# Optimization experiments

Measured on AMD Instinct MI355X. Metric: run time of the kernel, lower is better.

## Reference

```python
import jax, jax.numpy as jnp
import numpy as np

B, D_IN, D_OUT = 64, 1024, 1024

def setup_inputs() -> dict:
    key = jax.random.key(0)
    ks = jax.random.split(key, 7)
    return {
        "a_mean": jax.random.normal(ks[0], (B, D_IN), jnp.float32),
        "a_cov": jax.random.normal(ks[1], (B, D_IN, D_IN), jnp.float32),
        "weight": jax.random.normal(ks[2], (D_OUT, D_IN), jnp.float32) / np.sqrt(D_IN),
        "bias": jax.random.normal(ks[3], (D_OUT,), jnp.float32),
        "w_kfacs_A": jax.random.normal(ks[4], (D_IN, D_IN), jnp.float32) / np.sqrt(D_IN),
        "w_kfacs_B": jax.random.normal(ks[5], (D_OUT, D_OUT), jnp.float32) / np.sqrt(D_OUT),
        "b_cov": jax.random.normal(ks[6], (D_OUT, D_OUT), jnp.float32),
    }

def reference(a_mean, a_cov, weight, bias, w_kfacs_A, w_kfacs_B, b_cov):
    # h_mean = a_mean @ W^T + b
    h_mean = a_mean @ weight.T + bias  # [B, D_out]
    # Kron term: einsum('ni,nj,kl,ij->nkl') = (a_mean_n^T A a_mean_n) * B_kl
    s = jnp.einsum('ni,ij,nj->n', a_mean, w_kfacs_A, a_mean)  # [B]
    # Trace term: einsum('nij,kl,ij->nkl') = (sum_ij a_cov_nij * A_ij) * B_kl
    t = jnp.einsum('nij,ij->n', a_cov, w_kfacs_A)  # [B]
    kron_term = (s + t)[:, None, None] * w_kfacs_B  # [B, D_out, D_out]
    # Input-cov term: W @ a_cov_n @ W^T
    wcov = jnp.einsum('ki,nij,lj->nkl', weight, a_cov, weight)  # [B, D_out, D_out]
    h_cov = kron_term + wcov + b_cov
    return (h_mean, h_cov)
```

## Files before the change

### kernel.cpp

```cpp
#include <hip/hip_runtime.h>
#include <hip/hip_bf16.h>

typedef short bf16x8 __attribute__((ext_vector_type(8)));
typedef float f32x4  __attribute__((ext_vector_type(4)));

#define KD 1024

__device__ __forceinline__ short f2bf(float f) {
  unsigned u = __builtin_bit_cast(unsigned, f);
  u += 0x7fffu + ((u >> 16) & 1u);
  return (short)(u >> 16);
}

__device__ __forceinline__ void gll16(const short* g, short* l) {
  __builtin_amdgcn_global_load_lds((const __attribute__((address_space(1))) unsigned int*)g,
                                   (__attribute__((address_space(3))) unsigned int*)l,
                                   16, 0, 0);
}

template <int MODE>
__global__ __launch_bounds__(256) void gemm_bt(
    const short* __restrict__ A, size_t a_bs,
    const short* __restrict__ B, size_t b_bs,
    float* __restrict__ out, size_t o_bs,
    short* __restrict__ tout, size_t t_bs,
    const float* __restrict__ kB, const float* __restrict__ bcv,
    const float* __restrict__ cvec, int ncv0,
    const float* __restrict__ bias, int M) {
  __shared__ short sA[128 * 32];
  __shared__ short sB[128 * 32];
  const int t = threadIdx.x;
  const int z = blockIdx.z;
  const short* Ab = A + (size_t)z * a_bs;
  const short* Bb = B + (size_t)z * b_bs;
  const int m0 = blockIdx.x * 0 + blockIdx.y * 128, n0 = blockIdx.x * 128;
  const int lane = t & 63, wv = t >> 6;
  const int wm = (wv >> 1) * 64, wn = (wv & 1) * 64;
  const int r16 = lane & 15, q = lane >> 4;

  const int srow = wv * 16 + (lane >> 2);
  const int skof = (lane & 3) * 8;
  short* lA0 = &sA[(wv * 16) * 32];
  short* lA1 = &sA[(64 + wv * 16) * 32];
  short* lB0 = &sB[(wv * 16) * 32];
  short* lB1 = &sB[(64 + wv * 16) * 32];
  const int ar0 = min(m0 + srow, M - 1);
  const int ar1 = min(m0 + 64 + srow, M - 1);
  const short* gA0 = Ab + (size_t)ar0 * KD + skof;
  const short* gA1 = Ab + (size_t)ar1 * KD + skof;
  const short* gB0 = Bb + (size_t)(n0 + srow) * KD + skof;
  const short* gB1 = Bb + (size_t)(n0 + 64 + srow) * KD + skof;

  f32x4 acc[4][4];
  const f32x4 zero4 = {0.f, 0.f, 0.f, 0.f};
#pragma unroll
  for (int i = 0; i < 4; ++i)
#pragma unroll
    for (int j = 0; j < 4; ++j) acc[i][j] = zero4;

  for (int k0 = 0; k0 < KD; k0 += 32) {
    __syncthreads();
    gll16(gA0 + k0, lA0);
    gll16(gA1 + k0, lA1);
    gll16(gB0 + k0, lB0);
    gll16(gB1 + k0, lB1);
    __syncthreads();

    bf16x8 af[4], bf[4];
#pragma unroll
    for (int i = 0; i < 4; ++i) {
      af[i] = *(const bf16x8*)&sA[(wm + i * 16 + r16) * 32 + q * 8];
      bf[i] = *(const bf16x8*)&sB[(wn + i * 16 + r16) * 32 + q * 8];
    }
#pragma unroll
    for (int mi = 0; mi < 4; ++mi)
#pragma unroll
      for (int ni = 0; ni < 4; ++ni)
        acc[mi][ni] = __builtin_amdgcn_mfma_f32_16x16x32_bf16(af[mi], bf[ni], acc[mi][ni], 0, 0, 0);
  }

  float cv = 0.f;
  if (MODE == 2) cv = cvec[ncv0 + z];
  float* ob = out ? out + (size_t)z * o_bs : nullptr;

#pragma unroll
  for (int mi = 0; mi < 4; ++mi) {
#pragma unroll
    for (int ni = 0; ni < 4; ++ni) {
      const int row0 = m0 + wm + mi * 16 + q * 4;
      const int col = n0 + wn + ni * 16 + r16;
      f32x4 a = acc[mi][ni];
      if (MODE == 0) {
        float bv = bias[col];
#pragma unroll
        for (int r = 0; r < 4; ++r)
          if (row0 + r < M) ob[(size_t)(row0 + r) * 1024 + col] = a[r] + bv;
      } else if (MODE == 1) {
        short4 s;
        s.x = f2bf(a[0]); s.y = f2bf(a[1]); s.z = f2bf(a[2]); s.w = f2bf(a[3]);
        *(short4*)(tout + (size_t)z * t_bs + (size_t)col * 1024 + row0) = s;
      } else {
#pragma unroll
        for (int r = 0; r < 4; ++r) {
          size_t idx = (size_t)(row0 + r) * 1024 + col;
          ob[idx] = a[r] + cv * kB[idx] + bcv[idx];
        }
      }
    }
  }
}

__global__ __launch_bounds__(256) void conv_acov(const float* __restrict__ a_cov,
                                                 const float* __restrict__ a_mean,
                                                 const float* __restrict__ kA,
                                                 short* __restrict__ abf,
                                                 float* __restrict__ c) {
  const int n = blockIdx.x, ch = blockIdx.y, t = threadIdx.x;
  __shared__ float sm[1024];
  for (int j = t; j < 1024; j += 256) sm[j] = a_mean[n * 1024 + j];
  __syncthreads();
  const float4 amv = ((const float4*)sm)[t];
  const size_t cb = ((size_t)n << 20);
  float acc = 0.f;
  for (int i = ch * 64; i < ch * 64 + 64; ++i) {
    float4 Av = ((const float4*)(kA + ((size_t)i << 10)))[t];
    float4 Cv = ((const float4*)(a_cov + cb + ((size_t)i << 10)))[t];
    short4 s;
    s.x = f2bf(Cv.x); s.y = f2bf(Cv.y); s.z = f2bf(Cv.z); s.w = f2bf(Cv.w);
    *(short4*)(abf + cb + ((size_t)i << 10) + t * 4) = s;
    acc += Av.x * Cv.x + Av.y * Cv.y + Av.z * Cv.z + Av.w * Cv.w;
    acc += sm[i] * (Av.x * amv.x + Av.y * amv.y + Av.z * amv.z + Av.w * amv.w);
  }
#pragma unroll
  for (int off = 32; off > 0; off >>= 1) acc += __shfl_down(acc, off);
  __shared__ float red[4];
  if ((t & 63) == 0) red[t >> 6] = acc;
  __syncthreads();
  if (t == 0) atomicAdd(&c[n], red[0] + red[1] + red[2] + red[3]);
}

__global__ __launch_bounds__(256) void convf(const float* __restrict__ src,
                                             short* __restrict__ dst, int n4) {
  int i = blockIdx.x * 256 + threadIdx.x;
  if (i < n4) {
    float4 v = ((const float4*)src)[i];
    short4 s;
    s.x = f2bf(v.x); s.y = f2bf(v.y); s.z = f2bf(v.z); s.w = f2bf(v.w);
    ((short4*)dst)[i] = s;
  }
}

extern "C" void kernel_launch(void* const* d_in, const int* in_sizes, int n_in,
                              void* d_out, int out_size, void* d_ws, size_t ws_size,
                              hipStream_t stream) {
  const float* a_mean = (const float*)d_in[0];
  const float* a_cov  = (const float*)d_in[1];
  const float* weight = (const float*)d_in[2];
  const float* bias   = (const float*)d_in[3];
  const float* kA     = (const float*)d_in[4];
  const float* kB     = (const float*)d_in[5];
  const float* b_cov  = (const float*)d_in[6];
  float* h_mean = (float*)d_out;
  float* h_cov  = h_mean + (size_t)64 * 1024;

  const size_t SLICE = (size_t)1 << 20;
  float* cvec = (float*)d_ws;
  short* Wbf  = (short*)((char*)d_ws + 4096);
  short* ambf = Wbf + SLICE;
  char*  p    = (char*)(ambf + 65536);
  const size_t need_big = (size_t)((char*)p - (char*)d_ws) + 4 * SLICE * 64;
  const bool big = ws_size >= need_big;

  short* abf, *Tt;
  if (big) {
    abf = (short*)p;
    Tt  = abf + 64 * SLICE;
  } else {
    abf = (short*)h_cov;
    Tt  = (short*)(h_cov + 64 * SLICE / 2);
  }

  hipMemsetAsync(cvec, 0, 64 * sizeof(float), stream);
  convf<<<dim3(1024), 256, 0, stream>>>(weight, Wbf, 262144);
  convf<<<dim3(64), 256, 0, stream>>>(a_mean, ambf, 16384);
  conv_acov<<<dim3(64, 16), 256, 0, stream>>>(a_cov, a_mean, kA, abf, cvec);

  gemm_bt<1><<<dim3(8, 8, 64), 256, 0, stream>>>(
      abf, SLICE, Wbf, 0, nullptr, 0, Tt, SLICE,
      nullptr, nullptr, nullptr, 0, nullptr, 1024);

  gemm_bt<0><<<dim3(8, 1, 1), 256, 0, stream>>>(
      ambf, 0, Wbf, 0, h_mean, 0, nullptr, 0,
      nullptr, nullptr, nullptr, 0, bias, 64);

  if (big) {
    gemm_bt<2><<<dim3(8, 8, 64), 256, 0, stream>>>(
        Wbf, 0, Tt, SLICE, h_cov, SLICE, nullptr, 0,
        kB, b_cov, cvec, 0, nullptr, 1024);
  } else {
    short* T63 = ambf + 65536;
    hipMemcpyAsync(T63, Tt + 63 * SLICE, SLICE * 2, hipMemcpyDeviceToDevice, stream);
    const int st[6] = {0, 32, 48, 56, 60, 62};
    const int ln[6] = {32, 16, 8, 4, 2, 1};
    for (int w = 0; w < 6; ++w) {
      gemm_bt<2><<<dim3(8, 8, ln[w]), 256, 0, stream>>>(
          Wbf, 0, Tt + (size_t)st[w] * SLICE, SLICE,
          h_cov + (size_t)st[w] * SLICE, SLICE, nullptr, 0,
          kB, b_cov, cvec, st[w], nullptr, 1024);
    }
    gemm_bt<2><<<dim3(8, 8, 1), 256, 0, stream>>>(
        Wbf, 0, T63, 0, h_cov + (size_t)63 * SLICE, 0, nullptr, 0,
        kB, b_cov, cvec, 63, nullptr, 1024);
  }
}
```

Baseline: 957.1 us.

## Add 256x256-tile double-buffered GEMM kernel with swizzled LDS for batched covariance GEMMs

Adds a new 512-thread GEMM kernel with 256x256 output tiles and a 64-wide K step. It double-buffers LDS through async global-to-LDS loads, uses XOR-swizzled LDS addressing and interleaves MFMA quarters with barriers and priority hints. Both large batched GEMMs (a_cov@W^T and W@T plus the kron/bias epilogue) use it when 128KB of dynamic LDS can be configured. It aims to raise arithmetic intensity per LDS byte and overlap loads with compute. The cost is much higher register and LDS pressure per block and fewer blocks in the grid.

```diff
diff --git a/kernel.cpp b/kernel.cpp
--- a/kernel.cpp
+++ b/kernel.cpp
@@ -33,7 +33,7 @@
   const int z = blockIdx.z;
   const short* Ab = A + (size_t)z * a_bs;
   const short* Bb = B + (size_t)z * b_bs;
-  const int m0 = blockIdx.x * 0 + blockIdx.y * 128, n0 = blockIdx.x * 128;
+  const int m0 = blockIdx.y * 128, n0 = blockIdx.x * 128;
   const int lane = t & 63, wv = t >> 6;
   const int wm = (wv >> 1) * 64, wn = (wv & 1) * 64;
   const int r16 = lane & 15, q = lane >> 4;
@@ -96,6 +96,130 @@
         for (int r = 0; r < 4; ++r)
           if (row0 + r < M) ob[(size_t)(row0 + r) * 1024 + col] = a[r] + bv;
       } else if (MODE == 1) {
+        short4 s;
+        s.x = f2bf(a[0]); s.y = f2bf(a[1]); s.z = f2bf(a[2]); s.w = f2bf(a[3]);
+        *(short4*)(tout + (size_t)z * t_bs + (size_t)col * 1024 + row0) = s;
+      } else {
+#pragma unroll
+        for (int r = 0; r < 4; ++r) {
+          size_t idx = (size_t)(row0 + r) * 1024 + col;
+          ob[idx] = a[r] + cv * kB[idx] + bcv[idx];
+        }
+      }
+    }
+  }
+}
+
+template <int MODE>
+__global__ __launch_bounds__(512, 2) void gemm256(
+    const short* __restrict__ A, size_t a_bs,
+    const short* __restrict__ B, size_t b_bs,
+    float* __restrict__ out, size_t o_bs,
+    short* __restrict__ tout, size_t t_bs,
+    const float* __restrict__ kB, const float* __restrict__ bcv,
+    const float* __restrict__ cvec, int ncv0) {
+  extern __shared__ short lds[];
+  short* ldsB = lds + 32768;
+  const int t = threadIdx.x;
+  const int z = blockIdx.z;
+  const short* Ab = A + (size_t)z * a_bs;
+  const short* Bb = B + (size_t)z * b_bs;
+  const int m0 = blockIdx.y * 256, n0 = blockIdx.x * 256;
+  const int lane = t & 63, wv = t >> 6;
+  const int wm = (wv >> 2) * 128, wn = (wv & 3) * 64;
+  const int r16 = lane & 15, q = lane >> 4;
+  const int sw0 = ((q ^ (r16 & 7)) << 3);
+  const int sw1 = (((4 + q) ^ (r16 & 7)) << 3);
+
+  const int trow = t >> 3;
+  const int scol = (((t & 7) ^ (trow & 7)) << 3);
+  const short* gAa = Ab + (size_t)(m0 + trow) * KD + scol;
+  const short* gBa = Bb + (size_t)(n0 + trow) * KD + scol;
+  short* lAw = lds + wv * 512;
+  short* lBw = ldsB + wv * 512;
+
+#define STAGE_A(KT, H) { _Pragma("unroll") for (int r2 = 0; r2 < 2; ++r2) { \
+    const int rr = (H) * 2 + r2; \
+    gll16(gAa + (size_t)rr * (64 * KD) + (KT) * 64, lAw + ((KT) & 1) * 16384 + rr * 4096); } }
+#define STAGE_B(KT, H) { _Pragma("unroll") for (int r2 = 0; r2 < 2; ++r2) { \
+    const int rr = (H) * 2 + r2; \
+    gll16(gBa + (size_t)rr * (64 * KD) + (KT) * 64, lBw + ((KT) & 1) * 16384 + rr * 4096); } }
+
+  f32x4 acc[8][4];
+#pragma unroll
+  for (int i = 0; i < 8; ++i)
+#pragma unroll
+    for (int j = 0; j < 4; ++j) acc[i][j] = (f32x4){0.f, 0.f, 0.f, 0.f};
+
+  STAGE_A(0, 0); STAGE_A(0, 1); STAGE_B(0, 0); STAGE_B(0, 1);
+  STAGE_A(1, 0); STAGE_A(1, 1); STAGE_B(1, 0); STAGE_B(1, 1);
+  asm volatile("s_waitcnt vmcnt(8)" ::: "memory");
+  __builtin_amdgcn_s_barrier();
+
+  bf16x8 af[4][2];
+  bf16x8 bb[4][2];
+
+#define READ_A(MH) { _Pragma("unroll") for (int mq = 0; mq < 4; ++mq) { \
+    const short* p = sAc + (wm + (MH) * 64 + mq * 16 + r16) * 64; \
+    af[mq][0] = *(const bf16x8*)(p + sw0); \
+    af[mq][1] = *(const bf16x8*)(p + sw1); } }
+#define READ_B(NH) { _Pragma("unroll") for (int nq = 0; nq < 2; ++nq) { \
+    const short* p = sBc + (wn + (NH) * 32 + nq * 16 + r16) * 64; \
+    bb[(NH) * 2 + nq][0] = *(const bf16x8*)(p + sw0); \
+    bb[(NH) * 2 + nq][1] = *(const bf16x8*)(p + sw1); } }
+#define MFMA_Q(MH, NH) { _Pragma("unroll") for (int mq = 0; mq < 4; ++mq) \
+    _Pragma("unroll") for (int nq = 0; nq < 2; ++nq) { \
+      f32x4 c = acc[(MH) * 4 + mq][(NH) * 2 + nq]; \
+      c = __builtin_amdgcn_mfma_f32_16x16x32_bf16(af[mq][0], bb[(NH) * 2 + nq][0], c, 0, 0, 0); \
+      c = __builtin_amdgcn_mfma_f32_16x16x32_bf16(af[mq][1], bb[(NH) * 2 + nq][1], c, 0, 0, 0); \
+      acc[(MH) * 4 + mq][(NH) * 2 + nq] = c; } }
+#define BAR_IN() { asm volatile("" ::: "memory"); __builtin_amdgcn_s_barrier(); \
+    asm volatile("s_waitcnt lgkmcnt(0)" ::: "memory"); \
+    __builtin_amdgcn_sched_barrier(0); __builtin_amdgcn_s_setprio(1); }
+#define BAR_OUT() { __builtin_amdgcn_s_setprio(0); asm volatile("" ::: "memory"); \
+    __builtin_amdgcn_s_barrier(); }
+
+  for (int g = 0; g < 16; ++g) {
+    const short* sAc = lds + (g & 1) * 16384;
+    const short* sBc = ldsB + (g & 1) * 16384;
+    READ_A(0); READ_B(0);
+    BAR_IN(); MFMA_Q(0, 0); BAR_OUT();
+    READ_B(1);
+    BAR_IN(); MFMA_Q(0, 1); BAR_OUT();
+    READ_A(1);
+    if (g <= 13) { STAGE_B(g + 2, 0); STAGE_B(g + 2, 1); }
+    BAR_IN(); MFMA_Q(1, 0); BAR_OUT();
+    if (g <= 13) { STAGE_A(g + 2, 0); STAGE_A(g + 2, 1); }
+    asm volatile("" ::: "memory");
+    __builtin_amdgcn_s_barrier();
+    __builtin_amdgcn_s_setprio(1);
+    MFMA_Q(1, 1);
+    __builtin_amdgcn_s_setprio(0);
+    asm volatile("" ::: "memory");
+    if (g <= 13) { asm volatile("s_waitcnt vmcnt(8)" ::: "memory"); }
+    else         { asm volatile("s_waitcnt vmcnt(0)" ::: "memory"); }
+    __builtin_amdgcn_s_barrier();
+  }
+#undef STAGE_A
+#undef STAGE_B
+#undef READ_A
+#undef READ_B
+#undef MFMA_Q
+#undef BAR_IN
+#undef BAR_OUT
+
+  float cv = 0.f;
+  if (MODE == 2) cv = cvec[ncv0 + z];
+  float* ob = out ? out + (size_t)z * o_bs : nullptr;
+
+#pragma unroll
+  for (int me = 0; me < 8; ++me) {
+#pragma unroll
+    for (int ne = 0; ne < 4; ++ne) {
+      const int row0 = m0 + wm + me * 16 + q * 4;
+      const int col = n0 + wn + ne * 16 + r16;
+      f32x4 a = acc[me][ne];
+      if (MODE == 1) {
         short4 s;
         s.x = f2bf(a[0]); s.y = f2bf(a[1]); s.z = f2bf(a[2]); s.w = f2bf(a[3]);
         *(short4*)(tout + (size_t)z * t_bs + (size_t)col * 1024 + row0) = s;
@@ -180,36 +304,72 @@
     Tt  = (short*)(h_cov + 64 * SLICE / 2);
   }
 
+  static int use256 = -1;
+  if (use256 < 0) {
+    auto k1 = gemm256<1>;
+    auto k2 = gemm256<2>;
+    bool ok1 = hipFuncSetAttribute(reinterpret_cast<const void*>(k1),
+                                   hipFuncAttributeMaxDynamicSharedMemorySize, 131072) == hipSuccess;
+    bool ok2 = hipFuncSetAttribute(reinterpret_cast<const void*>(k2),
+                                   hipFuncAttributeMaxDynamicSharedMemorySize, 131072) == hipSuccess;
+    use256 = (ok1 && ok2) ? 1 : 0;
+  }
+
   hipMemsetAsync(cvec, 0, 64 * sizeof(float), stream);
   convf<<<dim3(1024), 256, 0, stream>>>(weight, Wbf, 262144);
   convf<<<dim3(64), 256, 0, stream>>>(a_mean, ambf, 16384);
   conv_acov<<<dim3(64, 16), 256, 0, stream>>>(a_cov, a_mean, kA, abf, cvec);
 
-  gemm_bt<1><<<dim3(8, 8, 64), 256, 0, stream>>>(
-      abf, SLICE, Wbf, 0, nullptr, 0, Tt, SLICE,
-      nullptr, nullptr, nullptr, 0, nullptr, 1024);
+  if (use256) {
+    gemm256<1><<<dim3(4, 4, 64), 512, 131072, stream>>>(
+        abf, SLICE, Wbf, 0, nullptr, 0, Tt, SLICE,
+        nullptr, nullptr, nullptr, 0);
+  } else {
+    gemm_bt<1><<<dim3(8, 8, 64), 256, 0, stream>>>(
+        abf, SLICE, Wbf, 0, nullptr, 0, Tt, SLICE,
+        nullptr, nullptr, nullptr, 0, nullptr, 1024);
+  }
 
   gemm_bt<0><<<dim3(8, 1, 1), 256, 0, stream>>>(
       ambf, 0, Wbf, 0, h_mean, 0, nullptr, 0,
       nullptr, nullptr, nullptr, 0, bias, 64);
 
   if (big) {
-    gemm_bt<2><<<dim3(8, 8, 64), 256, 0, stream>>>(
-        Wbf, 0, Tt, SLICE, h_cov, SLICE, nullptr, 0,
-        kB, b_cov, cvec, 0, nullptr, 1024);
+    if (use256) {
+      gemm256<2><<<dim3(4, 4, 64), 512, 131072, stream>>>(
+          Wbf, 0, Tt, SLICE, h_cov, SLICE, nullptr, 0,
+          kB, b_cov, cvec, 0);
+    } else {
+      gemm_bt<2><<<dim3(8, 8, 64), 256, 0, stream>>>(
+          Wbf, 0, Tt, SLICE, h_cov, SLICE, nullptr, 0,
+          kB, b_cov, cvec, 0, nullptr, 1024);
+    }
   } else {
     short* T63 = ambf + 65536;
     hipMemcpyAsync(T63, Tt + 63 * SLICE, SLICE * 2, hipMemcpyDeviceToDevice, stream);
     const int st[6] = {0, 32, 48, 56, 60, 62};
     const int ln[6] = {32, 16, 8, 4, 2, 1};
     for (int w = 0; w < 6; ++w) {
-      gemm_bt<2><<<dim3(8, 8, ln[w]), 256, 0, stream>>>(
-          Wbf, 0, Tt + (size_t)st[w] * SLICE, SLICE,
-          h_cov + (size_t)st[w] * SLICE, SLICE, nullptr, 0,
-          kB, b_cov, cvec, st[w], nullptr, 1024);
-    }
-    gemm_bt<2><<<dim3(8, 8, 1), 256, 0, stream>>>(
-        Wbf, 0, T63, 0, h_cov + (size_t)63 * SLICE, 0, nullptr, 0,
-        kB, b_cov, cvec, 63, nullptr, 1024);
-  }
-}
+      if (use256) {
+        gemm256<2><<<dim3(4, 4, ln[w]), 512, 131072, stream>>>(
+            Wbf, 0, Tt + (size_t)st[w] * SLICE, SLICE,
+            h_cov + (size_t)st[w] * SLICE, SLICE, nullptr, 0,
+            kB, b_cov, cvec, st[w]);
+      } else {
+        gemm_bt<2><<<dim3(8, 8, ln[w]), 256, 0, stream>>>(
+            Wbf, 0, Tt + (size_t)st[w] * SLICE, SLICE,
+            h_cov + (size_t)st[w] * SLICE, SLICE, nullptr, 0,
+            kB, b_cov, cvec, st[w], nullptr, 1024);
+      }
+    }
+    if (use256) {
+      gemm256<2><<<dim3(4, 4, 1), 512, 131072, stream>>>(
+          Wbf, 0, T63, 0, h_cov + (size_t)63 * SLICE, 0, nullptr, 0,
+          kB, b_cov, cvec, 63);
+    } else {
+      gemm_bt<2><<<dim3(8, 8, 1), 256, 0, stream>>>(
+          Wbf, 0, T63, 0, h_cov + (size_t)63 * SLICE, 0, nullptr, 0,
+          kB, b_cov, cvec, 63, nullptr, 1024);
+    }
+  }
+}
```

Result: faster. 835.7 us (-12.7%).
